# Performance work log

Hardware: AMD Instinct MI355X
Metric: run time of the kernel (lower is better)

## Reference

```python
import jax, jax.numpy as jnp
import numpy as np
import math

B, S, D, H = 2, 2048, 1024, 16
D_K = D // H


def setup_inputs() -> dict:
    key = jax.random.key(0)
    ks = jax.random.split(key, 9)
    scale = 0.02
    return {
        "query": jax.random.normal(ks[0], (B, S, D), dtype=jnp.float32),
        "key": jax.random.normal(ks[1], (B, S, D), dtype=jnp.float32),
        "value": jax.random.normal(ks[2], (B, S, D), dtype=jnp.float32),
        "padding_mask": jax.random.bernoulli(ks[3], 0.1, (B, 1, 1, S)),
        "Wq": jax.random.normal(ks[4], (D, D), dtype=jnp.float32) * scale,
        "bq": jnp.zeros((D,), dtype=jnp.float32),
        "Wk": jax.random.normal(ks[5], (D, D), dtype=jnp.float32) * scale,
        "bk": jnp.zeros((D,), dtype=jnp.float32),
        "Wv": jax.random.normal(ks[6], (D, D), dtype=jnp.float32) * scale,
        "bv": jnp.zeros((D,), dtype=jnp.float32),
        "Wo": jax.random.normal(ks[7], (D, D), dtype=jnp.float32) * scale,
        "bo": jnp.zeros((D,), dtype=jnp.float32),
    }


def reference(query, key, value, padding_mask, Wq, bq, Wk, bk, Wv, bv, Wo, bo):
    # projections -> [B, H, S, d_k]
    q = (query @ Wq + bq).reshape(B, S, H, D_K).transpose(0, 2, 1, 3)
    k = (key @ Wk + bk).reshape(B, S, H, D_K).transpose(0, 2, 1, 3)
    v = (value @ Wv + bv).reshape(B, S, H, D_K).transpose(0, 2, 1, 3)

    # scores: [B, H, S, S]
    scores = jnp.einsum("bhqd,bhkd->bhqk", q, k) / math.sqrt(D_K)

    # faithful to original: triu(scores, 1).bool() -> True where upper-tri score != 0,
    # masked positions get value 1e-10 (NOT -inf) before softmax
    causal_mask = jnp.triu(scores, k=1) != 0
    scores = jnp.where(causal_mask, jnp.float32(1e-10), scores)
    scores = jnp.where(padding_mask, jnp.float32(1e-10), scores)

    attn = jax.nn.softmax(scores, axis=-1)
    out = jnp.einsum("bhqk,bhkd->bhqd", attn, v)  # [B, H, S, d_k]
    out = out.transpose(0, 2, 1, 3).reshape(B, S, D)
    return out @ Wo + bo
```

## Files before the change

kernel.cpp:

```cpp
#include <hip/hip_runtime.h>
#include <hip/hip_bf16.h>
#include <cstdint>
#include <cstddef>

typedef __hip_bfloat16 bf16;
typedef __attribute__((ext_vector_type(8))) short short8;
typedef __attribute__((ext_vector_type(4))) short s4v;
typedef __attribute__((ext_vector_type(4))) float floatx4;

#define B_ 2
#define S_ 2048
#define D_ 1024
#define H_ 16
#define DK_ 64
#define M_ 4096
#define HEADELEMS 131072
#define TILEELEMS 4096
#define QSCALE 0.1803368801111204f

struct __align__(8) bf16x4 { bf16 x, y, z, w; };

__device__ __forceinline__ floatx4 mfma16(short8 a, short8 b, floatx4 c) {
  return __builtin_amdgcn_mfma_f32_16x16x32_bf16(a, b, c, 0, 0, 0);
}
__device__ __forceinline__ void gl_lds16(const bf16* g, bf16* l) {
  __builtin_amdgcn_global_load_lds((const __attribute__((address_space(1))) void*)g,
                                   (__attribute__((address_space(3))) void*)l, 16, 0, 0);
}
__device__ __forceinline__ float bs2f(short s) {
  bf16 b = *reinterpret_cast<bf16*>(&s);
  return __bfloat162float(b);
}
__device__ __forceinline__ s4v pack4(float p0, float p1, float p2, float p3) {
  union { __hip_bfloat162 h; short2 s; } ua, ub;
  ua.h = __float22bfloat162_rn(make_float2(p0, p1));
  ub.h = __float22bfloat162_rn(make_float2(p2, p3));
  s4v r = {ua.s.x, ua.s.y, ub.s.x, ub.s.y};
  return r;
}

__global__ void prep_kernel(const float* __restrict__ q_in, const float* __restrict__ k_in,
                            const float* __restrict__ v_in,
                            const float* __restrict__ Wq, const float* __restrict__ Wk,
                            const float* __restrict__ Wv, const float* __restrict__ Wo,
                            bf16* __restrict__ xq, bf16* __restrict__ xk, bf16* __restrict__ xv,
                            bf16* __restrict__ wqt, bf16* __restrict__ wkt,
                            bf16* __restrict__ wvt, bf16* __restrict__ wot,
                            const unsigned int* __restrict__ pmask, int* __restrict__ flag) {
  __shared__ bf16 tile[64][66];
  __shared__ int sbyte;
  const int blk = blockIdx.x;
  const int tid = threadIdx.x;
  if (blk < 12288) {
    const int z = blk >> 12;
    const int i = ((blk & 4095) << 8) | tid;
    const float* src = (z == 0) ? q_in : (z == 1) ? k_in : v_in;
    bf16* dst = (z == 0) ? xq : (z == 1) ? xk : xv;
    float4 v = ((const float4*)src)[i];
    bf16x4 o = { __float2bfloat16(v.x), __float2bfloat16(v.y),
                 __float2bfloat16(v.z), __float2bfloat16(v.w) };
    ((bf16x4*)dst)[i] = o;
  } else if (blk < 13312) {
    const int t = blk - 12288;
    const int z = t >> 8;
    const int rc = t & 255;
    const int r0 = (rc >> 4) * 64, c0 = (rc & 15) * 64;
    const float* src = (z == 0) ? Wq : (z == 1) ? Wk : (z == 2) ? Wv : Wo;
    bf16* dst = (z == 0) ? wqt : (z == 1) ? wkt : (z == 2) ? wvt : wot;
    const int lr = tid >> 4;
    const int lc4 = (tid & 15) * 4;
#pragma unroll
    for (int i = 0; i < 4; ++i) {
      const int r = lr + i * 16;
      float4 v = *(const float4*)(src + (size_t)(r0 + r) * D_ + c0 + lc4);
      tile[r][lc4 + 0] = __float2bfloat16(v.x);
      tile[r][lc4 + 1] = __float2bfloat16(v.y);
      tile[r][lc4 + 2] = __float2bfloat16(v.z);
      tile[r][lc4 + 3] = __float2bfloat16(v.w);
    }
    __syncthreads();
    const int orr = tid & 63;
    const int oc0 = tid >> 6;
#pragma unroll
    for (int j = 0; j < 16; ++j) {
      const int oc = oc0 + j * 4;
      dst[(size_t)(c0 + oc) * D_ + r0 + orr] = tile[orr][oc];
    }
  } else {
    if (tid == 0) sbyte = 0;
    __syncthreads();
    for (int i = tid; i < (B_ * S_) / 4; i += 256) {
      const unsigned int v = pmask[i];
      if (((v & 0xFEFEFEFEu) == 0u) && ((v & 0xFFFFFF00u) != 0u)) sbyte = 1;
    }
    __syncthreads();
    if (tid == 0) *flag = sbyte;
  }
}

template<int MT>
__global__ __launch_bounds__(256, 2) void gemm_k(
    const bf16* __restrict__ A0, const bf16* __restrict__ A1, const bf16* __restrict__ A2,
    const bf16* __restrict__ W0, const bf16* __restrict__ W1, const bf16* __restrict__ W2,
    const float* __restrict__ b0, const float* __restrict__ b1, const float* __restrict__ b2,
    void* __restrict__ O0, void* __restrict__ O1, void* __restrict__ O2,
    const int mode01, const int Kd, const float sc)
{
  __shared__ __align__(16) bf16 sh[(MT + 128) * 32];
  bf16* As = sh;
  bf16* Bs = sh + MT * 32;
  const int z = blockIdx.z;
  const bf16* A = (z == 0) ? A0 : (z == 1) ? A1 : A2;
  const bf16* W = (z == 0) ? W0 : (z == 1) ? W1 : W2;
  const float* bias = (z == 0) ? b0 : (z == 1) ? b1 : b2;
  void* Cout = (z == 0) ? O0 : (z == 1) ? O1 : O2;
  const int mode = (z == 2) ? 1 : mode01;
  const float scz = (z == 0) ? sc : 1.f;

  constexpr int MI = MT / 32;
  const int tid = threadIdx.x;
  const int wave = tid >> 6, lane = tid & 63;
  const int quad = lane >> 4, lc = lane & 15;
  const int wm = (wave >> 1) * (MT / 2), wn = (wave & 1) * 64;
  const int m0 = blockIdx.y * MT, n0 = blockIdx.x * 128;

  const floatx4 zero4 = {0.f, 0.f, 0.f, 0.f};
  floatx4 acc[MI][4];
#pragma unroll
  for (int mi = 0; mi < MI; ++mi)
#pragma unroll
    for (int ni = 0; ni < 4; ++ni) acc[mi][ni] = zero4;

  const int ldr = lane >> 2;
  const int ldc = (lane & 3) * 8;
  const bf16* Ag = A + (size_t)(m0 + wave * (MT / 4) + ldr) * Kd + ldc;
  const bf16* Bg = W + (size_t)(n0 + wave * 32 + ldr) * Kd + ldc;
  bf16* As0 = As + wave * (MT / 4) * 32;
  bf16* Bs0 = Bs + wave * 32 * 32;

  for (int k0 = 0; k0 < Kd; k0 += 32) {
    gl_lds16(Ag + k0, As0);
    if (MT == 128) gl_lds16(Ag + k0 + (size_t)16 * Kd, As0 + 16 * 32);
    gl_lds16(Bg + k0, Bs0);
    gl_lds16(Bg + k0 + (size_t)16 * Kd, Bs0 + 16 * 32);
    __syncthreads();

    short8 af[MI], bfr[4];
#pragma unroll
    for (int i = 0; i < MI; ++i)
      af[i] = *(const short8*)(As + (wm + i * 16 + lc) * 32 + quad * 8);
#pragma unroll
    for (int i = 0; i < 4; ++i)
      bfr[i] = *(const short8*)(Bs + (wn + i * 16 + lc) * 32 + quad * 8);
#pragma unroll
    for (int mi = 0; mi < MI; ++mi)
#pragma unroll
      for (int ni = 0; ni < 4; ++ni)
        acc[mi][ni] = mfma16(af[mi], bfr[ni], acc[mi][ni]);
    __syncthreads();
  }

  if (mode == 2) {
    float* out = (float*)Cout;
#pragma unroll
    for (int mi = 0; mi < MI; ++mi)
#pragma unroll
      for (int ni = 0; ni < 4; ++ni) {
        const int col = n0 + wn + ni * 16 + lc;
        const float bv = bias[col];
        const int rbase = m0 + wm + mi * 16 + quad * 4;
#pragma unroll
        for (int r = 0; r < 4; ++r)
          out[(size_t)(rbase + r) * D_ + col] = acc[mi][ni][r] + bv;
      }
  } else {
    bf16* pool = sh + wave * 2048;
    float bvs[4];
#pragma unroll
    for (int ni = 0; ni < 4; ++ni) bvs[ni] = bias[n0 + wn + ni * 16 + lc];
    const int hcol = (n0 + wn) >> 6;
    const int mglob = m0 + wm;
    bf16* outb = (bf16*)Cout + (size_t)((mglob >> 11) * H_ + hcol) * HEADELEMS
               + (size_t)((mglob & (S_ - 1)) >> 6) * TILEELEMS;
#pragma unroll
    for (int half = 0; half < MI / 2; ++half) {
#pragma unroll
      for (int mi2 = 0; mi2 < 2; ++mi2) {
        const int mi = half * 2 + mi2;
#pragma unroll
        for (int ni = 0; ni < 4; ++ni) {
          const int dkl = ni * 16 + lc;
#pragma unroll
          for (int r = 0; r < 4; ++r) {
            const float v = (acc[mi][ni][r] + bvs[ni]) * scz;
            int idx;
            if (mode == 0) {
              const int c = (mi2 * 2 + (dkl >> 5)) * 64 + ((dkl >> 3) & 3) * 16 + quad * 4 + r;
              idx = c * 8 + (dkl & 7);
            } else {
              const int c = (mi2 * 4 + (dkl >> 4)) * 64 + quad * 16 + (dkl & 15);
              idx = c * 4 + r;
            }
            pool[idx] = __float2bfloat16(v);
          }
        }
      }
#pragma unroll
      for (int t = 0; t < 4; ++t) {
        const short8 vv = *(const short8*)(pool + t * 512 + lane * 8);
        *(short8*)(outb + half * 2048 + t * 512 + lane * 8) = vv;
      }
    }
  }
}

__global__ void suf_kernel(const bf16* __restrict__ vp, float* __restrict__ suf) {
  __shared__ float ts[32 * 64];
  const int bhid = blockIdx.x;
  const bf16* vb = vp + (size_t)bhid * HEADELEMS;
  const int tid = threadIdx.x;
  const int dk = tid & 63, g = tid >> 6;
  const int dkt = dk >> 4, lck = dk & 15;
  for (int T = g * 8; T < g * 8 + 8; ++T) {
    float sum = 0.f;
#pragma unroll
    for (int w = 0; w < 4; ++w)
#pragma unroll
      for (int qd = 0; qd < 4; ++qd) {
        const s4v x = *(const s4v*)(vb + (size_t)T * TILEELEMS
                                    + (size_t)(((w * 4 + dkt) * 64 + qd * 16 + lck)) * 4);
        sum += bs2f(x[0]) + bs2f(x[1]) + bs2f(x[2]) + bs2f(x[3]);
      }
    ts[T * 64 + dk] = sum;
  }
  __syncthreads();
  if (g == 0) {
    float run = 0.f;
    float* out = suf + (size_t)bhid * (33 * 64);
    out[32 * 64 + dk] = 0.f;
    for (int T = 31; T >= 0; --T) { run += ts[T * 64 + dk]; out[T * 64 + dk] = run; }
  }
}

__device__ __forceinline__ void load_pad(const void* pad, int bytemode, int idx, bool pm[4]) {
  if (bytemode) {
    const uchar4 u = *(const uchar4*)((const unsigned char*)pad + idx);
    pm[0] = u.x != 0; pm[1] = u.y != 0; pm[2] = u.z != 0; pm[3] = u.w != 0;
  } else {
    const int4 u = *(const int4*)((const int*)pad + idx);
    pm[0] = u.x != 0; pm[1] = u.y != 0; pm[2] = u.z != 0; pm[3] = u.w != 0;
  }
}

__device__ __forceinline__ void qk_tile(const short8 ak0, const short8 ak1,
                                        const short8 (&qf)[4][2],
                                        const bool pm[4], float (&lacc)[4], s4v (&pf)[4],
                                        const int w, const int quad, const int lc,
                                        const bool diag) {
  const floatx4 z4 = {0.f, 0.f, 0.f, 0.f};
  const short ONE = (short)0x3F80;
#pragma unroll
  for (int qt = 0; qt < 4; ++qt) {
    if (diag && w > qt) {
      s4v o1 = {ONE, ONE, ONE, ONE};
      pf[qt] = o1;
      lacc[qt] += 4.f;
      continue;
    }
    floatx4 s = mfma16(ak0, qf[qt][0], z4);
    s = mfma16(ak1, qf[qt][1], s);
    float pv[4];
#pragma unroll
    for (int r = 0; r < 4; ++r) {
      bool m = pm[r];
      if (diag && w == qt) m = m || (quad * 4 + r > lc);
      pv[r] = exp2f(m ? 0.f : s[r]);
      lacc[qt] += pv[r];
    }
    pf[qt] = pack4(pv[0], pv[1], pv[2], pv[3]);
  }
}

__global__ __launch_bounds__(256, 2) void attn_kernel(
    const bf16* __restrict__ qp, const bf16* __restrict__ kp,
    const bf16* __restrict__ vp, const float* __restrict__ suf,
    const void* __restrict__ pad, const int* __restrict__ flag,
    bf16* __restrict__ oa)
{
  __shared__ __align__(16) bf16 smem[12800];
  __shared__ float lbuf[256];

  const int lin = blockIdx.x;
  const int xcd = lin & 7;
  const int i2 = lin >> 3;
  const int grp = i2 >> 5;
  const int r5 = i2 & 31;
  const int bh = xcd + 8 * grp;
  const int rr = (grp & 2) ? ((r5 + 16) & 31) : r5;
  const int myqt = (grp & 1) ? rr : (31 - rr);
  const int b = bh >> 4, h = bh & 15;

  const int mynt = myqt + 1;
  const int mynp = (mynt + 1) >> 1;
  const int tid = threadIdx.x;
  const int w = tid >> 6, lane = tid & 63, quad = lane >> 4, lc = lane & 15;
  const int bytemode = *flag;
  const int padbase = b * S_;

  const bf16* qb = qp + (size_t)bh * HEADELEMS + (size_t)myqt * TILEELEMS;
  short8 qf[4][2];
#pragma unroll
  for (int qt = 0; qt < 4; ++qt)
#pragma unroll
    for (int hh = 0; hh < 2; ++hh)
      qf[qt][hh] = *(const short8*)(qb + (size_t)((qt * 2 + hh) * 64 + lane) * 8);

  const bf16* kwp = kp + (size_t)bh * HEADELEMS + (size_t)(w * 128 + lane) * 8;
  const bf16* vwp = vp + (size_t)bh * HEADELEMS + (size_t)(w * 4 * 64 + lane) * 4;

  const floatx4 zero4 = {0.f, 0.f, 0.f, 0.f};
  floatx4 oacc[4][4];
#pragma unroll
  for (int i = 0; i < 4; ++i)
#pragma unroll
    for (int jj = 0; jj < 4; ++jj) oacc[i][jj] = zero4;
  float lacc[4] = {0.f, 0.f, 0.f, 0.f};

  for (int p = 0; p < mynp; ++p) {
    const int T0 = 2 * p, T1 = 2 * p + 1;
    const size_t o0 = (size_t)T0 * TILEELEMS, o1 = o0 + TILEELEMS;
    const short8 ak00 = *(const short8*)(kwp + o0);
    const short8 ak01 = *(const short8*)(kwp + o0 + 512);
    const short8 ak10 = *(const short8*)(kwp + o1);
    const short8 ak11 = *(const short8*)(kwp + o1 + 512);
    s4v va0[4], va1[4];
#pragma unroll
    for (int dkt = 0; dkt < 4; ++dkt) {
      va0[dkt] = *(const s4v*)(vwp + o0 + dkt * 256);
      va1[dkt] = *(const s4v*)(vwp + o1 + dkt * 256);
    }

    bool pm[4];
    s4v pf0[4], pf1[4];
    load_pad(pad, bytemode, padbase + T0 * 64 + w * 16 + quad * 4, pm);
    qk_tile(ak00, ak01, qf, pm, lacc, pf0, w, quad, lc, T0 == mynt - 1);
    if (T1 < mynt) {
      load_pad(pad, bytemode, padbase + T1 * 64 + w * 16 + quad * 4, pm);
      qk_tile(ak10, ak11, qf, pm, lacc, pf1, w, quad, lc, T1 == mynt - 1);
    } else {
      const s4v zz = {0, 0, 0, 0};
#pragma unroll
      for (int qt = 0; qt < 4; ++qt) pf1[qt] = zz;
    }

    short8 pB[4];
#pragma unroll
    for (int qt = 0; qt < 4; ++qt)
      pB[qt] = __builtin_shufflevector(pf0[qt], pf1[qt], 0, 1, 2, 3, 4, 5, 6, 7);
#pragma unroll
    for (int dkt = 0; dkt < 4; ++dkt) {
      const short8 av = __builtin_shufflevector(va0[dkt], va1[dkt], 0, 1, 2, 3, 4, 5, 6, 7);
#pragma unroll
      for (int qt = 0; qt < 4; ++qt)
        oacc[dkt][qt] = mfma16(av, pB[qt], oacc[dkt][qt]);
    }
  }

#pragma unroll
  for (int qt = 0; qt < 4; ++qt) {
    float v = lacc[qt];
    v += __shfl_xor(v, 16);
    v += __shfl_xor(v, 32);
    if (quad == 0) lbuf[w * 64 + qt * 16 + lc] = v;
  }
  __syncthreads();
  float* fbuf = (float*)smem;
  bf16* obuf = smem + 8192;
  float ls = lbuf[0 * 64 + w * 16 + lc] + lbuf[1 * 64 + w * 16 + lc]
           + lbuf[2 * 64 + w * 16 + lc] + lbuf[3 * 64 + w * 16 + lc];
  ls += (float)(S_ - mynt * 64);
  const float linv = 1.f / ls;
  const float* sufp = suf + (size_t)bh * (33 * 64) + mynt * 64;

#pragma unroll
  for (int dktG = 0; dktG < 4; ++dktG) {
#pragma unroll
    for (int qt = 0; qt < 4; ++qt) {
      const floatx4 a = oacc[dktG][qt];
      float* dst = fbuf + (w * 4 + qt) * 256 + lc;
#pragma unroll
      for (int r = 0; r < 4; ++r) dst[(quad * 4 + r) * 16] = a[r];
    }
    __syncthreads();
    const float4 sv4 = *(const float4*)(sufp + dktG * 16 + quad * 4);
    float v[4];
#pragma unroll
    for (int r = 0; r < 4; ++r) {
      const int e = (quad * 4 + r) * 16 + lc;
      v[r] = fbuf[(0 * 4 + w) * 256 + e] + fbuf[(1 * 4 + w) * 256 + e]
           + fbuf[(2 * 4 + w) * 256 + e] + fbuf[(3 * 4 + w) * 256 + e];
    }
    v[0] = (v[0] + sv4.x) * linv; v[1] = (v[1] + sv4.y) * linv;
    v[2] = (v[2] + sv4.z) * linv; v[3] = (v[3] + sv4.w) * linv;
    bf16x4 pk = { __float2bfloat16(v[0]), __float2bfloat16(v[1]),
                  __float2bfloat16(v[2]), __float2bfloat16(v[3]) };
    *(bf16x4*)(obuf + (w * 16 + lc) * 72 + dktG * 16 + quad * 4) = pk;
    __syncthreads();
  }

  const size_t obase = (size_t)(b * S_ + myqt * 64) * D_ + h * 64;
#pragma unroll
  for (int it = 0; it < 2; ++it) {
    const int idx = it * 256 + tid;
    const int row = idx >> 3, c8 = (idx & 7) * 8;
    const short8 vv = *(const short8*)(obuf + row * 72 + c8);
    *(short8*)(oa + obase + (size_t)row * D_ + c8) = vv;
  }
}

extern "C" void kernel_launch(void* const* d_in, const int* in_sizes, int n_in,
                              void* d_out, int out_size, void* d_ws, size_t ws_size,
                              hipStream_t stream) {
  (void)in_sizes; (void)n_in; (void)out_size; (void)ws_size;
  const float* q_in = (const float*)d_in[0];
  const float* k_in = (const float*)d_in[1];
  const float* v_in = (const float*)d_in[2];
  const void*  pmask = d_in[3];
  const float* Wq = (const float*)d_in[4];
  const float* bq = (const float*)d_in[5];
  const float* Wk = (const float*)d_in[6];
  const float* bk = (const float*)d_in[7];
  const float* Wv = (const float*)d_in[8];
  const float* bv = (const float*)d_in[9];
  const float* Wo = (const float*)d_in[10];
  const float* bo = (const float*)d_in[11];

  char* ws = (char*)d_ws;
  bf16* xq  = (bf16*)(ws + 0);
  bf16* xk  = (bf16*)(ws + 8388608);
  bf16* xv  = (bf16*)(ws + 16777216);
  bf16* wqt = (bf16*)(ws + 25165824);
  bf16* wkt = (bf16*)(ws + 27262976);
  bf16* wvt = (bf16*)(ws + 29360128);
  bf16* wot = (bf16*)(ws + 31457280);
  bf16* qpp = (bf16*)(ws + 33554432);
  bf16* kpp = (bf16*)(ws + 41943040);
  bf16* vpp = (bf16*)(ws + 50331648);
  float* suf = (float*)(ws + 25165824);
  int*  flg = (int*)(ws + 58720256);
  bf16* oa  = xq;

  prep_kernel<<<13313, 256, 0, stream>>>(q_in, k_in, v_in, Wq, Wk, Wv, Wo,
                                         xq, xk, xv, wqt, wkt, wvt, wot,
                                         (const unsigned int*)pmask, flg);

  gemm_k<128><<<dim3(8, 32, 3), 256, 0, stream>>>(xq, xk, xv, wqt, wkt, wvt,
                                                  bq, bk, bv, qpp, kpp, vpp, 0, D_, QSCALE);
  suf_kernel<<<32, 256, 0, stream>>>(vpp, suf);

  attn_kernel<<<1024, 256, 0, stream>>>(qpp, kpp, vpp, suf, pmask, flg, oa);

  gemm_k<64><<<dim3(8, 64, 1), 256, 0, stream>>>(oa, oa, oa, wot, wot, wot,
                                                 bo, bo, bo, d_out, d_out, d_out, 2, D_, 1.f);
}
```

Measured before the change: 247.0 us.

## Pair causal query tiles per block and software-pipeline K/V loads in attention

```diff
diff --git a/kernel.cpp b/kernel.cpp
--- a/kernel.cpp
+++ b/kernel.cpp
@@ -37,6 +37,13 @@
   ub.h = __float22bfloat162_rn(make_float2(p2, p3));
   s4v r = {ua.s.x, ua.s.y, ub.s.x, ub.s.y};
   return r;
+}
+__device__ __forceinline__ float fast_exp2(float x) {
+#if __has_builtin(__builtin_amdgcn_exp2f)
+  return __builtin_amdgcn_exp2f(x);
+#else
+  float r; asm("v_exp_f32 %0, %1" : "=v"(r) : "v"(x)); return r;
+#endif
 }
 
 __global__ void prep_kernel(const float* __restrict__ q_in, const float* __restrict__ k_in,
@@ -252,6 +259,30 @@
   }
 }
 
+struct KVF {
+  short8 ak00, ak01, ak10, ak11;
+  s4v va0[4], va1[4];
+  bool pm0[4], pm1[4];
+};
+
+__device__ __forceinline__ void load_kv(const bf16* kwp, const bf16* vwp,
+                                        const void* pad, const int bytemode,
+                                        const int pidx, const int p, KVF& f) {
+  const size_t o0 = (size_t)(2 * p) * TILEELEMS, o1 = o0 + TILEELEMS;
+  f.ak00 = *(const short8*)(kwp + o0);
+  f.ak01 = *(const short8*)(kwp + o0 + 512);
+  f.ak10 = *(const short8*)(kwp + o1);
+  f.ak11 = *(const short8*)(kwp + o1 + 512);
+#pragma unroll
+  for (int dkt = 0; dkt < 4; ++dkt) {
+    f.va0[dkt] = *(const s4v*)(vwp + o0 + dkt * 256);
+    f.va1[dkt] = *(const s4v*)(vwp + o1 + dkt * 256);
+  }
+  load_pad(pad, bytemode, pidx + 2 * p * 64, f.pm0);
+  load_pad(pad, bytemode, pidx + (2 * p + 1) * 64, f.pm1);
+}
+
+template<bool DIAGP>
 __device__ __forceinline__ void qk_tile(const short8 ak0, const short8 ak1,
                                         const short8 (&qf)[4][2],
                                         const bool pm[4], float (&lacc)[4], s4v (&pf)[4],
@@ -261,7 +292,7 @@
   const short ONE = (short)0x3F80;
 #pragma unroll
   for (int qt = 0; qt < 4; ++qt) {
-    if (diag && w > qt) {
+    if (DIAGP && diag && w > qt) {
       s4v o1 = {ONE, ONE, ONE, ONE};
       pf[qt] = o1;
       lacc[qt] += 4.f;
@@ -273,148 +304,152 @@
 #pragma unroll
     for (int r = 0; r < 4; ++r) {
       bool m = pm[r];
-      if (diag && w == qt) m = m || (quad * 4 + r > lc);
-      pv[r] = exp2f(m ? 0.f : s[r]);
+      if (DIAGP && diag && w == qt) m = m || (quad * 4 + r > lc);
+      pv[r] = fast_exp2(m ? 0.f : s[r]);
       lacc[qt] += pv[r];
     }
     pf[qt] = pack4(pv[0], pv[1], pv[2], pv[3]);
   }
 }
 
-__global__ __launch_bounds__(256, 2) void attn_kernel(
+__device__ __forceinline__ void pv_step(const KVF& f, const s4v (&pf0)[4], const s4v (&pf1)[4],
+                                        floatx4 (&oacc)[4][4]) {
+  short8 pB[4];
+#pragma unroll
+  for (int qt = 0; qt < 4; ++qt)
+    pB[qt] = __builtin_shufflevector(pf0[qt], pf1[qt], 0, 1, 2, 3, 4, 5, 6, 7);
+#pragma unroll
+  for (int dkt = 0; dkt < 4; ++dkt) {
+    const short8 av = __builtin_shufflevector(f.va0[dkt], f.va1[dkt], 0, 1, 2, 3, 4, 5, 6, 7);
+#pragma unroll
+    for (int qt = 0; qt < 4; ++qt)
+      oacc[dkt][qt] = mfma16(av, pB[qt], oacc[dkt][qt]);
+  }
+}
+
+__global__ __launch_bounds__(256, 1) void attn_kernel(
     const bf16* __restrict__ qp, const bf16* __restrict__ kp,
     const bf16* __restrict__ vp, const float* __restrict__ suf,
     const void* __restrict__ pad, const int* __restrict__ flag,
     bf16* __restrict__ oa)
 {
-  __shared__ __align__(16) bf16 smem[12800];
+  __shared__ __align__(16) bf16 smem[13312];
   __shared__ float lbuf[256];
 
   const int lin = blockIdx.x;
   const int xcd = lin & 7;
-  const int i2 = lin >> 3;
-  const int grp = i2 >> 5;
-  const int r5 = i2 & 31;
+  const int t = lin >> 3;
+  const int grp = t >> 4;
+  const int jq = t & 15;
   const int bh = xcd + 8 * grp;
-  const int rr = (grp & 2) ? ((r5 + 16) & 31) : r5;
-  const int myqt = (grp & 1) ? rr : (31 - rr);
   const int b = bh >> 4, h = bh & 15;
 
-  const int mynt = myqt + 1;
-  const int mynp = (mynt + 1) >> 1;
   const int tid = threadIdx.x;
   const int w = tid >> 6, lane = tid & 63, quad = lane >> 4, lc = lane & 15;
   const int bytemode = *flag;
-  const int padbase = b * S_;
-
-  const bf16* qb = qp + (size_t)bh * HEADELEMS + (size_t)myqt * TILEELEMS;
-  short8 qf[4][2];
-#pragma unroll
-  for (int qt = 0; qt < 4; ++qt)
-#pragma unroll
-    for (int hh = 0; hh < 2; ++hh)
-      qf[qt][hh] = *(const short8*)(qb + (size_t)((qt * 2 + hh) * 64 + lane) * 8);
+  const int pidx = b * S_ + w * 16 + quad * 4;
 
   const bf16* kwp = kp + (size_t)bh * HEADELEMS + (size_t)(w * 128 + lane) * 8;
   const bf16* vwp = vp + (size_t)bh * HEADELEMS + (size_t)(w * 4 * 64 + lane) * 4;
 
-  const floatx4 zero4 = {0.f, 0.f, 0.f, 0.f};
-  floatx4 oacc[4][4];
-#pragma unroll
-  for (int i = 0; i < 4; ++i)
-#pragma unroll
-    for (int jj = 0; jj < 4; ++jj) oacc[i][jj] = zero4;
-  float lacc[4] = {0.f, 0.f, 0.f, 0.f};
-
-  for (int p = 0; p < mynp; ++p) {
-    const int T0 = 2 * p, T1 = 2 * p + 1;
-    const size_t o0 = (size_t)T0 * TILEELEMS, o1 = o0 + TILEELEMS;
-    const short8 ak00 = *(const short8*)(kwp + o0);
-    const short8 ak01 = *(const short8*)(kwp + o0 + 512);
-    const short8 ak10 = *(const short8*)(kwp + o1);
-    const short8 ak11 = *(const short8*)(kwp + o1 + 512);
-    s4v va0[4], va1[4];
-#pragma unroll
-    for (int dkt = 0; dkt < 4; ++dkt) {
-      va0[dkt] = *(const s4v*)(vwp + o0 + dkt * 256);
-      va1[dkt] = *(const s4v*)(vwp + o1 + dkt * 256);
-    }
-
-    bool pm[4];
-    s4v pf0[4], pf1[4];
-    load_pad(pad, bytemode, padbase + T0 * 64 + w * 16 + quad * 4, pm);
-    qk_tile(ak00, ak01, qf, pm, lacc, pf0, w, quad, lc, T0 == mynt - 1);
-    if (T1 < mynt) {
-      load_pad(pad, bytemode, padbase + T1 * 64 + w * 16 + quad * 4, pm);
-      qk_tile(ak10, ak11, qf, pm, lacc, pf1, w, quad, lc, T1 == mynt - 1);
-    } else {
-      const s4v zz = {0, 0, 0, 0};
-#pragma unroll
-      for (int qt = 0; qt < 4; ++qt) pf1[qt] = zz;
-    }
-
-    short8 pB[4];
+#pragma unroll 1
+  for (int qsel = 0; qsel < 2; ++qsel) {
+    const int myqt = qsel ? jq : 31 - jq;
+    const int mynt = myqt + 1;
+    const int pfull = (mynt - 1) >> 1;
+
+    const bf16* qb = qp + (size_t)bh * HEADELEMS + (size_t)myqt * TILEELEMS;
+    short8 qf[4][2];
 #pragma unroll
     for (int qt = 0; qt < 4; ++qt)
-      pB[qt] = __builtin_shufflevector(pf0[qt], pf1[qt], 0, 1, 2, 3, 4, 5, 6, 7);
-#pragma unroll
-    for (int dkt = 0; dkt < 4; ++dkt) {
-      const short8 av = __builtin_shufflevector(va0[dkt], va1[dkt], 0, 1, 2, 3, 4, 5, 6, 7);
-#pragma unroll
-      for (int qt = 0; qt < 4; ++qt)
-        oacc[dkt][qt] = mfma16(av, pB[qt], oacc[dkt][qt]);
-    }
-  }
-
-#pragma unroll
-  for (int qt = 0; qt < 4; ++qt) {
-    float v = lacc[qt];
-    v += __shfl_xor(v, 16);
-    v += __shfl_xor(v, 32);
-    if (quad == 0) lbuf[w * 64 + qt * 16 + lc] = v;
-  }
-  __syncthreads();
-  float* fbuf = (float*)smem;
-  bf16* obuf = smem + 8192;
-  float ls = lbuf[0 * 64 + w * 16 + lc] + lbuf[1 * 64 + w * 16 + lc]
-           + lbuf[2 * 64 + w * 16 + lc] + lbuf[3 * 64 + w * 16 + lc];
-  ls += (float)(S_ - mynt * 64);
-  const float linv = 1.f / ls;
-  const float* sufp = suf + (size_t)bh * (33 * 64) + mynt * 64;
-
-#pragma unroll
-  for (int dktG = 0; dktG < 4; ++dktG) {
+#pragma unroll
+      for (int hh = 0; hh < 2; ++hh)
+        qf[qt][hh] = *(const short8*)(qb + (size_t)((qt * 2 + hh) * 64 + lane) * 8);
+
+    const floatx4 zero4 = {0.f, 0.f, 0.f, 0.f};
+    floatx4 oacc[4][4];
+#pragma unroll
+    for (int i = 0; i < 4; ++i)
+#pragma unroll
+      for (int jj = 0; jj < 4; ++jj) oacc[i][jj] = zero4;
+    float lacc[4] = {0.f, 0.f, 0.f, 0.f};
+
+    KVF f;
+    load_kv(kwp, vwp, pad, bytemode, pidx, 0, f);
+#pragma unroll 1
+    for (int p = 0; p < pfull; ++p) {
+      KVF fn;
+      load_kv(kwp, vwp, pad, bytemode, pidx, p + 1, fn);
+      s4v pf0[4], pf1[4];
+      qk_tile<false>(f.ak00, f.ak01, qf, f.pm0, lacc, pf0, w, quad, lc, false);
+      qk_tile<false>(f.ak10, f.ak11, qf, f.pm1, lacc, pf1, w, quad, lc, false);
+      pv_step(f, pf0, pf1, oacc);
+      f = fn;
+    }
+    {
+      const int T0 = 2 * pfull, T1 = T0 + 1;
+      s4v pf0[4], pf1[4];
+      qk_tile<true>(f.ak00, f.ak01, qf, f.pm0, lacc, pf0, w, quad, lc, T0 == mynt - 1);
+      if (T1 < mynt) {
+        qk_tile<true>(f.ak10, f.ak11, qf, f.pm1, lacc, pf1, w, quad, lc, T1 == mynt - 1);
+      } else {
+        const s4v zz = {0, 0, 0, 0};
+#pragma unroll
+        for (int qt = 0; qt < 4; ++qt) pf1[qt] = zz;
+      }
+      pv_step(f, pf0, pf1, oacc);
+    }
+
 #pragma unroll
     for (int qt = 0; qt < 4; ++qt) {
-      const floatx4 a = oacc[dktG][qt];
-      float* dst = fbuf + (w * 4 + qt) * 256 + lc;
-#pragma unroll
-      for (int r = 0; r < 4; ++r) dst[(quad * 4 + r) * 16] = a[r];
+      float v = lacc[qt];
+      v += __shfl_xor(v, 16);
+      v += __shfl_xor(v, 32);
+      if (quad == 0) lbuf[w * 64 + qt * 16 + lc] = v;
     }
     __syncthreads();
-    const float4 sv4 = *(const float4*)(sufp + dktG * 16 + quad * 4);
-    float v[4];
-#pragma unroll
-    for (int r = 0; r < 4; ++r) {
-      const int e = (quad * 4 + r) * 16 + lc;
-      v[r] = fbuf[(0 * 4 + w) * 256 + e] + fbuf[(1 * 4 + w) * 256 + e]
-           + fbuf[(2 * 4 + w) * 256 + e] + fbuf[(3 * 4 + w) * 256 + e];
-    }
-    v[0] = (v[0] + sv4.x) * linv; v[1] = (v[1] + sv4.y) * linv;
-    v[2] = (v[2] + sv4.z) * linv; v[3] = (v[3] + sv4.w) * linv;
-    bf16x4 pk = { __float2bfloat16(v[0]), __float2bfloat16(v[1]),
-                  __float2bfloat16(v[2]), __float2bfloat16(v[3]) };
-    *(bf16x4*)(obuf + (w * 16 + lc) * 72 + dktG * 16 + quad * 4) = pk;
-    __syncthreads();
-  }
-
-  const size_t obase = (size_t)(b * S_ + myqt * 64) * D_ + h * 64;
-#pragma unroll
-  for (int it = 0; it < 2; ++it) {
-    const int idx = it * 256 + tid;
-    const int row = idx >> 3, c8 = (idx & 7) * 8;
-    const short8 vv = *(const short8*)(obuf + row * 72 + c8);
-    *(short8*)(oa + obase + (size_t)row * D_ + c8) = vv;
+    float* fbuf = (float*)smem;
+    bf16* obuf = smem + 8704;
+    float ls = lbuf[0 * 64 + w * 16 + lc] + lbuf[1 * 64 + w * 16 + lc]
+             + lbuf[2 * 64 + w * 16 + lc] + lbuf[3 * 64 + w * 16 + lc];
+    ls += (float)(S_ - mynt * 64);
+    const float linv = 1.f / ls;
+    const float* sufp = suf + (size_t)bh * (33 * 64) + mynt * 64;
+
+#pragma unroll
+    for (int dktG = 0; dktG < 4; ++dktG) {
+#pragma unroll
+      for (int qt = 0; qt < 4; ++qt) {
+        const floatx4 a = oacc[dktG][qt];
+        float* dst = fbuf + (w * 4 + qt) * 272 + lc;
+#pragma unroll
+        for (int r = 0; r < 4; ++r) dst[(quad * 4 + r) * 17] = a[r];
+      }
+      __syncthreads();
+      const float4 sv4 = *(const float4*)(sufp + dktG * 16 + quad * 4);
+      float v[4];
+#pragma unroll
+      for (int r = 0; r < 4; ++r) {
+        const int e = (quad * 4 + r) * 17 + lc;
+        v[r] = fbuf[(0 * 4 + w) * 272 + e] + fbuf[(1 * 4 + w) * 272 + e]
+             + fbuf[(2 * 4 + w) * 272 + e] + fbuf[(3 * 4 + w) * 272 + e];
+      }
+      v[0] = (v[0] + sv4.x) * linv; v[1] = (v[1] + sv4.y) * linv;
+      v[2] = (v[2] + sv4.z) * linv; v[3] = (v[3] + sv4.w) * linv;
+      bf16x4 pk = { __float2bfloat16(v[0]), __float2bfloat16(v[1]),
+                    __float2bfloat16(v[2]), __float2bfloat16(v[3]) };
+      *(bf16x4*)(obuf + (w * 16 + lc) * 72 + dktG * 16 + quad * 4) = pk;
+      __syncthreads();
+    }
+
+    const size_t obase = (size_t)(b * S_ + myqt * 64) * D_ + h * 64;
+#pragma unroll
+    for (int it = 0; it < 2; ++it) {
+      const int idx = it * 256 + tid;
+      const int row = idx >> 3, c8 = (idx & 7) * 8;
+      const short8 vv = *(const short8*)(obuf + row * 72 + c8);
+      *(short8*)(oa + obase + (size_t)row * D_ + c8) = vv;
+    }
   }
 }
 
@@ -458,7 +493,7 @@
                                                   bq, bk, bv, qpp, kpp, vpp, 0, D_, QSCALE);
   suf_kernel<<<32, 256, 0, stream>>>(vpp, suf);
 
-  attn_kernel<<<1024, 256, 0, stream>>>(qpp, kpp, vpp, suf, pmask, flg, oa);
+  attn_kernel<<<512, 256, 0, stream>>>(qpp, kpp, vpp, suf, pmask, flg, oa);
 
   gemm_k<64><<<dim3(8, 64, 1), 256, 0, stream>>>(oa, oa, oa, wot, wot, wot,
                                                  bo, bo, bo, d_out, d_out, d_out, 2, D_, 1.f);
```

New measurement: 249.7 us. No clear change (+1.1%).
